# Performance work log

Hardware: AMD Instinct MI355X
Metric: run time of the kernel (lower is better)

## Reference

```python
import jax, jax.numpy as jnp
import numpy as np

B, N, C, E = 8, 4096, 128, 131072  # batch, nodes, channels (in==out), edges


def _linear_params(key, fan_in, fan_out):
    kw, kb = jax.random.split(key)
    s = 1.0 / np.sqrt(fan_in).astype(np.float32)
    W = jax.random.uniform(kw, (fan_in, fan_out), jnp.float32, -s, s)
    b = jax.random.uniform(kb, (fan_out,), jnp.float32, -s, s)
    return W, b


def setup_inputs() -> dict:
    key = jax.random.key(0)
    ks = jax.random.split(key, 6)
    x = jax.random.normal(ks[0], (B, N, C), jnp.float32)
    edge_index = jax.random.randint(ks[1], (2, E), 0, N, jnp.int64)
    W0, b0 = _linear_params(ks[2], C, C)        # lin0: in -> out
    W1, b1 = _linear_params(ks[3], 2 * C, C)    # lin1: 2*out -> out
    W2, b2 = _linear_params(ks[4], C, C)        # lin2: out -> out
    Wo, bo = _linear_params(ks[5], C, C)        # output: out -> out
    return {"x": x, "edge_index": edge_index, "W0": W0, "b0": b0,
            "W1": W1, "b1": b1, "W2": W2, "b2": b2, "Wo": Wo, "bo": bo}


def reference(x, edge_index, W0, b0, W1, b1, W2, b2, Wo, bo):
    n = x.shape[1]
    # symmetric 0/1 adjacency (duplicate edges collapse via .set), zero diagonal
    adj = jnp.zeros((n, n), x.dtype)
    adj = adj.at[edge_index[0], edge_index[1]].set(1.0)
    adj = adj.at[edge_index[1], edge_index[0]].set(1.0)
    diag = jnp.arange(n)
    adj = adj.at[diag, diag].set(0.0)
    h = x @ W0 + b0                               # [B, N, C]
    agg = jnp.einsum('ij,bjd->bid', adj, h)       # neighbor aggregation
    cat = jnp.concatenate([x, agg], axis=-1)      # [B, N, 2C]
    out = (cat @ W1 + b1) @ W2 + b2
    out = jax.nn.gelu(out, approximate=False) @ Wo + bo  # torch exact GELU
    return x + out
```

## Files before the change

### kernel.cpp

```cpp
#include <hip/hip_runtime.h>
#include <hip/hip_bf16.h>
#include <math.h>

#define NN 4096
#define BB 8
#define CC 128
#define EE 131072
#define M_ROWS (BB*NN)
#define DEG_CAP 512

typedef __attribute__((ext_vector_type(8))) short short8;
typedef __attribute__((ext_vector_type(4))) float f32x4;

__device__ __forceinline__ float bf2f(unsigned int u){
    union { unsigned int i; float f; } v; v.i = u << 16; return v.f;
}
__device__ __forceinline__ unsigned short f2bf(float f){
    union { float f; unsigned int i; } v; v.f = f;
    unsigned int u = v.i;
    unsigned int r = u + 0x7FFFu + ((u >> 16) & 1u);
    return (unsigned short)(r >> 16);
}

__device__ __forceinline__ int swz(int r, int k2 ){
    return r * 256 + (k2 ^ ((r & 7) << 4));
}

__global__ __launch_bounds__(256) void k_prep_w(const float* __restrict__ W0, const float* __restrict__ W1,
                                                const float* __restrict__ W2, const float* __restrict__ Wo,
                                                unsigned short* __restrict__ Wt0, unsigned short* __restrict__ Wt1a,
                                                unsigned short* __restrict__ Wt1b, unsigned short* __restrict__ Wt2,
                                                unsigned short* __restrict__ Wto){
    int idx = blockIdx.x * blockDim.x + threadIdx.x;
    int s = idx >> 14;
    int e = idx & 16383;
    int n = e >> 7, k = e & 127;
    float v; unsigned short* dst;
    switch (s){
        case 0:  v = W0[k*128+n];        dst = Wt0;  break;
        case 1:  v = W1[k*128+n];        dst = Wt1a; break;
        case 2:  v = W1[(128+k)*128+n];  dst = Wt1b; break;
        case 3:  v = W2[k*128+n];        dst = Wt2;  break;
        default: v = Wo[k*128+n];        dst = Wto;  break;
    }
    dst[n*128+k] = f2bf(v);
}

__global__ __launch_bounds__(256) void k_scatter(const int* __restrict__ ei,
                                                 unsigned char* __restrict__ adj){
    int e = blockIdx.x * blockDim.x + threadIdx.x;
    if (e < EE){
        int u = ei[e], v = ei[EE + e];
        adj[(size_t)u * NN + v] = 1;
        adj[(size_t)v * NN + u] = 1;
    }
}

__global__ __launch_bounds__(256) void k_csr(const unsigned char* __restrict__ adj,
                                             int* __restrict__ cols, int* __restrict__ deg){
    __shared__ int sc[256];
    int i = blockIdx.x, t = threadIdx.x;
    uint4 w = *((const uint4*)(adj + (size_t)i * NN + t * 16));
    unsigned char b[16]; *((uint4*)b) = w;
    int c = 0;
    #pragma unroll
    for (int q = 0; q < 16; q++){ int j = t*16 + q; if (b[q] && j != i) c++; }
    sc[t] = c; __syncthreads();
    int val = c;
    for (int off = 1; off < 256; off <<= 1){
        int add = (t >= off) ? sc[t - off] : 0;
        __syncthreads();
        val += add; sc[t] = val;
        __syncthreads();
    }
    int total = sc[255];
    int pos = val - c;
    #pragma unroll
    for (int q = 0; q < 16; q++){
        int j = t*16 + q;
        if (b[q] && j != i){
            if (pos < DEG_CAP) cols[(size_t)i * DEG_CAP + pos] = j;
            pos++;
        }
    }
    if (t == 0) deg[i] = total < DEG_CAP ? total : DEG_CAP;
}

__global__ __launch_bounds__(256) void k_agg(const unsigned short* __restrict__ hT,
                                             const int* __restrict__ cols,
                                             const int* __restrict__ deg,
                                             unsigned short* __restrict__ aggbf){
    int i = blockIdx.x, t = threadIdx.x;
    int d = deg[i];
    const int* cl = cols + (size_t)i * DEG_CAP;
    const unsigned short* hp = hT + t * 4;
    float a0 = 0.f, a1 = 0.f, a2 = 0.f, a3 = 0.f;
    int n = 0;
    for (; n + 3 < d; n += 4){
        int4 c = *((const int4*)(cl + n));
        uint2 u0 = *((const uint2*)(hp + ((size_t)c.x << 10)));
        uint2 u1 = *((const uint2*)(hp + ((size_t)c.y << 10)));
        uint2 u2 = *((const uint2*)(hp + ((size_t)c.z << 10)));
        uint2 u3 = *((const uint2*)(hp + ((size_t)c.w << 10)));
        a0 += bf2f(u0.x & 0xFFFFu) + bf2f(u1.x & 0xFFFFu) + bf2f(u2.x & 0xFFFFu) + bf2f(u3.x & 0xFFFFu);
        a1 += bf2f(u0.x >> 16)     + bf2f(u1.x >> 16)     + bf2f(u2.x >> 16)     + bf2f(u3.x >> 16);
        a2 += bf2f(u0.y & 0xFFFFu) + bf2f(u1.y & 0xFFFFu) + bf2f(u2.y & 0xFFFFu) + bf2f(u3.y & 0xFFFFu);
        a3 += bf2f(u0.y >> 16)     + bf2f(u1.y >> 16)     + bf2f(u2.y >> 16)     + bf2f(u3.y >> 16);
    }
    for (; n < d; ++n){
        int j0 = cl[n];
        uint2 u0 = *((const uint2*)(hp + ((size_t)j0 << 10)));
        a0 += bf2f(u0.x & 0xFFFFu);
        a1 += bf2f(u0.x >> 16);
        a2 += bf2f(u0.y & 0xFFFFu);
        a3 += bf2f(u0.y >> 16);
    }
    int b  = t >> 5;
    int ch = (t & 31) * 4;
    ushort4 o; o.x = f2bf(a0); o.y = f2bf(a1); o.z = f2bf(a2); o.w = f2bf(a3);
    *((ushort4*)(aggbf + (size_t)b * (NN*128) + (size_t)i * 128 + ch)) = o;
}

__device__ __forceinline__ void stage_a_bf16(const unsigned short* __restrict__ src, int blockRow,
                                             unsigned short* As, int t){
    #pragma unroll
    for (int it = 0; it < 4; ++it){
        int g = it * 2048 + t * 8;
        int r = g >> 7, k = g & 127;
        uint4 v = *((const uint4*)(src + (size_t)(blockRow + r) * 128 + k));
        *((uint4*)((char*)As + swz(r, k * 2))) = v;
    }
}
__device__ __forceinline__ void stage_a_f32(const float* __restrict__ src, int blockRow,
                                            unsigned short* As, int t){
    #pragma unroll
    for (int it = 0; it < 4; ++it){
        int g = it * 2048 + t * 8;
        int r = g >> 7, k = g & 127;
        const float* p = src + (size_t)(blockRow + r) * 128 + k;
        float4 lo = *((const float4*)p);
        float4 hi = *((const float4*)(p + 4));
        ushort4 w0, w1;
        w0.x = f2bf(lo.x); w0.y = f2bf(lo.y); w0.z = f2bf(lo.z); w0.w = f2bf(lo.w);
        w1.x = f2bf(hi.x); w1.y = f2bf(hi.y); w1.z = f2bf(hi.z); w1.w = f2bf(hi.w);
        char* dst = (char*)As + swz(r, k * 2);
        *((ushort4*)dst) = w0;
        *((ushort4*)(dst + 8)) = w1;
    }
}
__device__ __forceinline__ void stage_w(const unsigned short* __restrict__ Wt,
                                        unsigned short* Ws, int t){
    #pragma unroll
    for (int it = 0; it < 8; ++it){
        int g = it * 2048 + t * 8;
        int r = g >> 7, k = g & 127;
        uint4 v = *((const uint4*)(Wt + r * 128 + k));
        *((uint4*)((char*)Ws + swz(r, k * 2))) = v;
    }
}
__device__ __forceinline__ void mfma_pass(const unsigned short* As, const unsigned short* Ws,
                                          int wr, int wc, int l15, int lh, f32x4 acc[2][4]){
    #pragma unroll
    for (int ks = 0; ks < 4; ++ks){
        const int kc = ks * 32 + lh * 8;
        short8 af[2], bfv[4];
        #pragma unroll
        for (int m = 0; m < 2; m++){
            int r = wr + m * 16 + l15;
            af[m] = *((const short8*)((const char*)As + swz(r, kc * 2)));
        }
        #pragma unroll
        for (int n = 0; n < 4; n++){
            int r = wc + n * 16 + l15;
            bfv[n] = *((const short8*)((const char*)Ws + swz(r, kc * 2)));
        }
        #pragma unroll
        for (int m = 0; m < 2; m++)
            #pragma unroll
            for (int n = 0; n < 4; n++)
                acc[m][n] = __builtin_amdgcn_mfma_f32_16x16x32_bf16(af[m], bfv[n], acc[m][n], 0, 0, 0);
    }
}

__global__ __launch_bounds__(256) void k_gemm0(const float* __restrict__ x,
                                               const unsigned short* __restrict__ Wt0,
                                               const float* __restrict__ b0,
                                               unsigned short* __restrict__ hT){
    __shared__ unsigned short As[64*128];
    __shared__ unsigned short Ws[128*128];
    const int t = threadIdx.x;
    const int blockRow = blockIdx.x * 64;
    stage_a_f32(x, blockRow, As, t);
    stage_w(Wt0, Ws, t);
    __syncthreads();
    const int lane = t & 63, w = t >> 6;
    const int wr = (w >> 1) * 32, wc = (w & 1) * 64;
    const int l15 = lane & 15, lh = lane >> 4;
    f32x4 acc[2][4];
    #pragma unroll
    for (int m = 0; m < 2; m++) for (int n = 0; n < 4; n++) acc[m][n] = (f32x4)(0.0f);
    mfma_pass(As, Ws, wr, wc, l15, lh, acc);
    #pragma unroll
    for (int m = 0; m < 2; m++){
        #pragma unroll
        for (int rr = 0; rr < 4; rr++){
            int row = blockRow + wr + m * 16 + lh * 4 + rr;
            int b_ = row >> 12, j = row & 4095;
            #pragma unroll
            for (int n = 0; n < 4; n++){
                int col = wc + n * 16 + l15;
                float v = acc[m][n][rr] + b0[col];
                hT[(size_t)j * 1024 + b_ * 128 + col] = f2bf(v);
            }
        }
    }
}

__global__ __launch_bounds__(256) void k_gemm1(const float* __restrict__ x,
                                               const unsigned short* __restrict__ agg,
                                               const unsigned short* __restrict__ Wt1a,
                                               const unsigned short* __restrict__ Wt1b,
                                               const float* __restrict__ b1,
                                               unsigned short* __restrict__ t1bf){
    __shared__ unsigned short As[64*128];
    __shared__ unsigned short Ws[128*128];
    const int t = threadIdx.x;
    const int blockRow = blockIdx.x * 64;
    const int lane = t & 63, w = t >> 6;
    const int wr = (w >> 1) * 32, wc = (w & 1) * 64;
    const int l15 = lane & 15, lh = lane >> 4;
    f32x4 acc[2][4];
    #pragma unroll
    for (int m = 0; m < 2; m++) for (int n = 0; n < 4; n++) acc[m][n] = (f32x4)(0.0f);

    stage_a_f32(x, blockRow, As, t);
    stage_w(Wt1a, Ws, t);
    __syncthreads();
    mfma_pass(As, Ws, wr, wc, l15, lh, acc);
    __syncthreads();
    stage_a_bf16(agg, blockRow, As, t);
    stage_w(Wt1b, Ws, t);
    __syncthreads();
    mfma_pass(As, Ws, wr, wc, l15, lh, acc);

    #pragma unroll
    for (int m = 0; m < 2; m++){
        #pragma unroll
        for (int rr = 0; rr < 4; rr++){
            int row = blockRow + wr + m * 16 + lh * 4 + rr;
            #pragma unroll
            for (int n = 0; n < 4; n++){
                int col = wc + n * 16 + l15;
                float v = acc[m][n][rr] + b1[col];
                t1bf[(size_t)row * 128 + col] = f2bf(v);
            }
        }
    }
}

__global__ __launch_bounds__(256) void k_gemm23(const unsigned short* __restrict__ t1bf,
                                                const unsigned short* __restrict__ Wt2,
                                                const unsigned short* __restrict__ Wto,
                                                const float* __restrict__ b2,
                                                const float* __restrict__ bo,
                                                const float* __restrict__ x,
                                                float* __restrict__ out){
    __shared__ unsigned short As[64*128];
    __shared__ unsigned short Ws2[128*128];
    __shared__ unsigned short Wso[128*128];
    const int t = threadIdx.x;
    const int blockRow = blockIdx.x * 64;
    const int lane = t & 63, w = t >> 6;
    const int wr = (w >> 1) * 32, wc = (w & 1) * 64;
    const int l15 = lane & 15, lh = lane >> 4;

    stage_a_bf16(t1bf, blockRow, As, t);
    stage_w(Wt2, Ws2, t);
    stage_w(Wto, Wso, t);
    __syncthreads();

    f32x4 acc[2][4];
    #pragma unroll
    for (int m = 0; m < 2; m++) for (int n = 0; n < 4; n++) acc[m][n] = (f32x4)(0.0f);
    mfma_pass(As, Ws2, wr, wc, l15, lh, acc);
    __syncthreads();

    #pragma unroll
    for (int m = 0; m < 2; m++){
        #pragma unroll
        for (int rr = 0; rr < 4; rr++){
            int rl = wr + m * 16 + lh * 4 + rr;
            #pragma unroll
            for (int n = 0; n < 4; n++){
                int col = wc + n * 16 + l15;
                float v = acc[m][n][rr] + b2[col];
                v = 0.5f * v * (1.0f + erff(v * 0.70710678118f));
                *((unsigned short*)((char*)As + swz(rl, col * 2))) = f2bf(v);
            }
        }
    }
    __syncthreads();

    f32x4 acc2[2][4];
    #pragma unroll
    for (int m = 0; m < 2; m++) for (int n = 0; n < 4; n++) acc2[m][n] = (f32x4)(0.0f);
    mfma_pass(As, Wso, wr, wc, l15, lh, acc2);

    #pragma unroll
    for (int m = 0; m < 2; m++){
        #pragma unroll
        for (int rr = 0; rr < 4; rr++){
            int row = blockRow + wr + m * 16 + lh * 4 + rr;
            #pragma unroll
            for (int n = 0; n < 4; n++){
                int col = wc + n * 16 + l15;
                float v = acc2[m][n][rr] + bo[col] + x[(size_t)row * 128 + col];
                out[(size_t)row * 128 + col] = v;
            }
        }
    }
}

extern "C" void kernel_launch(void* const* d_in, const int* in_sizes, int n_in,
                              void* d_out, int out_size, void* d_ws, size_t ws_size,
                              hipStream_t stream) {
    const float* x  = (const float*)d_in[0];
    const int*   ei = (const int*)d_in[1];
    const float* W0 = (const float*)d_in[2];
    const float* b0 = (const float*)d_in[3];
    const float* W1 = (const float*)d_in[4];
    const float* b1 = (const float*)d_in[5];
    const float* W2 = (const float*)d_in[6];
    const float* b2 = (const float*)d_in[7];
    const float* Wo = (const float*)d_in[8];
    const float* bo = (const float*)d_in[9];
    float* out = (float*)d_out;

    char* ws = (char*)d_ws;
    unsigned char* adj   = (unsigned char*)(ws + 0);
    int*   cols          = (int*)(ws + 16777216);
    int*   deg           = (int*)(ws + 25165824);
    unsigned short* hT   = (unsigned short*)(ws + 25182208);
    unsigned short* aggb = (unsigned short*)(ws + 33570816);
    unsigned short* t1bf = (unsigned short*)(ws + 41959424);
    unsigned short* Wt0  = (unsigned short*)(ws + 50348032);
    unsigned short* Wt1a = (unsigned short*)(ws + 50348032 + 32768);
    unsigned short* Wt1b = (unsigned short*)(ws + 50348032 + 65536);
    unsigned short* Wt2  = (unsigned short*)(ws + 50348032 + 98304);
    unsigned short* Wto  = (unsigned short*)(ws + 50348032 + 131072);

    hipMemsetAsync(adj, 0, (size_t)NN * NN, stream);

    k_prep_w<<<320, 256, 0, stream>>>(W0, W1, W2, Wo, Wt0, Wt1a, Wt1b, Wt2, Wto);
    k_scatter<<<EE / 256, 256, 0, stream>>>(ei, adj);
    k_csr<<<NN, 256, 0, stream>>>(adj, cols, deg);

    k_gemm0<<<M_ROWS / 64, 256, 0, stream>>>(x, Wt0, b0, hT);
    k_agg<<<NN, 256, 0, stream>>>(hT, cols, deg, aggb);
    k_gemm1<<<M_ROWS / 64, 256, 0, stream>>>(x, aggb, Wt1a, Wt1b, b1, t1bf);
    k_gemm23<<<M_ROWS / 64, 256, 0, stream>>>(t1bf, Wt2, Wto, b2, bo, x, out);
}
```

Baseline: 93.80 us.

## Use bitset adjacency with atomicOr and widen aggregation loads

Replaces the 16 MB byte adjacency matrix with a 2 MB bitset built via atomicOr, so the memset and the CSR pass read far less memory; CSR build now uses popcount and ffs over 32-bit words. The aggregation kernel stages column indices in shared memory, uses 16-byte loads covering 8 channels per thread, splits neighbors across two thread halves, and reduces through shared memory. Atomics add contention on the scatter step, and the extra sync and reduction add overhead in the aggregation kernel.

```diff
diff --git a/kernel.cpp b/kernel.cpp
--- a/kernel.cpp
+++ b/kernel.cpp
@@ -47,78 +47,98 @@
 }
 
 __global__ __launch_bounds__(256) void k_scatter(const int* __restrict__ ei,
-                                                 unsigned char* __restrict__ adj){
+                                                 unsigned int* __restrict__ bits){
     int e = blockIdx.x * blockDim.x + threadIdx.x;
     if (e < EE){
         int u = ei[e], v = ei[EE + e];
-        adj[(size_t)u * NN + v] = 1;
-        adj[(size_t)v * NN + u] = 1;
-    }
-}
-
-__global__ __launch_bounds__(256) void k_csr(const unsigned char* __restrict__ adj,
+        atomicOr(&bits[u * 128 + (v >> 5)], 1u << (v & 31));
+        atomicOr(&bits[v * 128 + (u >> 5)], 1u << (u & 31));
+    }
+}
+
+__global__ __launch_bounds__(128) void k_csr(const unsigned int* __restrict__ bits,
                                              int* __restrict__ cols, int* __restrict__ deg){
-    __shared__ int sc[256];
+    __shared__ int sc[128];
     int i = blockIdx.x, t = threadIdx.x;
-    uint4 w = *((const uint4*)(adj + (size_t)i * NN + t * 16));
-    unsigned char b[16]; *((uint4*)b) = w;
-    int c = 0;
-    #pragma unroll
-    for (int q = 0; q < 16; q++){ int j = t*16 + q; if (b[q] && j != i) c++; }
+    unsigned int w = bits[i * 128 + t];
+    if (t == (i >> 5)) w &= ~(1u << (i & 31));
+    int c = __popc(w);
     sc[t] = c; __syncthreads();
     int val = c;
-    for (int off = 1; off < 256; off <<= 1){
+    for (int off = 1; off < 128; off <<= 1){
         int add = (t >= off) ? sc[t - off] : 0;
         __syncthreads();
         val += add; sc[t] = val;
         __syncthreads();
     }
-    int total = sc[255];
+    int total = sc[127];
     int pos = val - c;
-    #pragma unroll
-    for (int q = 0; q < 16; q++){
-        int j = t*16 + q;
-        if (b[q] && j != i){
-            if (pos < DEG_CAP) cols[(size_t)i * DEG_CAP + pos] = j;
-            pos++;
-        }
+    unsigned int ww = w;
+    while (ww){
+        int b = __ffs(ww) - 1;
+        ww &= ww - 1;
+        if (pos < DEG_CAP) cols[(size_t)i * DEG_CAP + pos] = t * 32 + b;
+        pos++;
     }
     if (t == 0) deg[i] = total < DEG_CAP ? total : DEG_CAP;
+}
+
+__device__ __forceinline__ void acc8(uint4 u, float* a){
+    a[0] += bf2f(u.x & 0xFFFFu); a[1] += bf2f(u.x >> 16);
+    a[2] += bf2f(u.y & 0xFFFFu); a[3] += bf2f(u.y >> 16);
+    a[4] += bf2f(u.z & 0xFFFFu); a[5] += bf2f(u.z >> 16);
+    a[6] += bf2f(u.w & 0xFFFFu); a[7] += bf2f(u.w >> 16);
 }
 
 __global__ __launch_bounds__(256) void k_agg(const unsigned short* __restrict__ hT,
                                              const int* __restrict__ cols,
                                              const int* __restrict__ deg,
                                              unsigned short* __restrict__ aggbf){
-    int i = blockIdx.x, t = threadIdx.x;
-    int d = deg[i];
+    __shared__ int scol[DEG_CAP];
+    __shared__ float red[128][9];
+    const int i = blockIdx.x, t = threadIdx.x;
+    const int half = t >> 7, lane = t & 127;
+    const int d = deg[i];
     const int* cl = cols + (size_t)i * DEG_CAP;
-    const unsigned short* hp = hT + t * 4;
-    float a0 = 0.f, a1 = 0.f, a2 = 0.f, a3 = 0.f;
-    int n = 0;
-    for (; n + 3 < d; n += 4){
-        int4 c = *((const int4*)(cl + n));
-        uint2 u0 = *((const uint2*)(hp + ((size_t)c.x << 10)));
-        uint2 u1 = *((const uint2*)(hp + ((size_t)c.y << 10)));
-        uint2 u2 = *((const uint2*)(hp + ((size_t)c.z << 10)));
-        uint2 u3 = *((const uint2*)(hp + ((size_t)c.w << 10)));
-        a0 += bf2f(u0.x & 0xFFFFu) + bf2f(u1.x & 0xFFFFu) + bf2f(u2.x & 0xFFFFu) + bf2f(u3.x & 0xFFFFu);
-        a1 += bf2f(u0.x >> 16)     + bf2f(u1.x >> 16)     + bf2f(u2.x >> 16)     + bf2f(u3.x >> 16);
-        a2 += bf2f(u0.y & 0xFFFFu) + bf2f(u1.y & 0xFFFFu) + bf2f(u2.y & 0xFFFFu) + bf2f(u3.y & 0xFFFFu);
-        a3 += bf2f(u0.y >> 16)     + bf2f(u1.y >> 16)     + bf2f(u2.y >> 16)     + bf2f(u3.y >> 16);
-    }
-    for (; n < d; ++n){
-        int j0 = cl[n];
-        uint2 u0 = *((const uint2*)(hp + ((size_t)j0 << 10)));
-        a0 += bf2f(u0.x & 0xFFFFu);
-        a1 += bf2f(u0.x >> 16);
-        a2 += bf2f(u0.y & 0xFFFFu);
-        a3 += bf2f(u0.y >> 16);
-    }
-    int b  = t >> 5;
-    int ch = (t & 31) * 4;
-    ushort4 o; o.x = f2bf(a0); o.y = f2bf(a1); o.z = f2bf(a2); o.w = f2bf(a3);
-    *((ushort4*)(aggbf + (size_t)b * (NN*128) + (size_t)i * 128 + ch)) = o;
+    for (int q = t; q < d; q += 256) scol[q] = cl[q];
+    __syncthreads();
+
+    const unsigned short* hp = hT + lane * 8;
+    float a[8];
+    #pragma unroll
+    for (int c = 0; c < 8; c++) a[c] = 0.f;
+
+    int n = half;
+    for (; n + 6 < d; n += 8){
+        int j0 = scol[n], j1 = scol[n+2], j2 = scol[n+4], j3 = scol[n+6];
+        uint4 u0 = *((const uint4*)(hp + ((size_t)j0 << 10)));
+        uint4 u1 = *((const uint4*)(hp + ((size_t)j1 << 10)));
+        uint4 u2 = *((const uint4*)(hp + ((size_t)j2 << 10)));
+        uint4 u3 = *((const uint4*)(hp + ((size_t)j3 << 10)));
+        acc8(u0, a); acc8(u1, a); acc8(u2, a); acc8(u3, a);
+    }
+    for (; n < d; n += 2){
+        uint4 u0 = *((const uint4*)(hp + ((size_t)scol[n] << 10)));
+        acc8(u0, a);
+    }
+
+    if (half){
+        #pragma unroll
+        for (int c = 0; c < 8; c++) red[lane][c] = a[c];
+    }
+    __syncthreads();
+    if (!half){
+        #pragma unroll
+        for (int c = 0; c < 8; c++) a[c] += red[lane][c];
+        int b  = lane >> 4;
+        int ch = (lane * 8) & 127;
+        uint4 o;
+        o.x = (unsigned)f2bf(a[0]) | ((unsigned)f2bf(a[1]) << 16);
+        o.y = (unsigned)f2bf(a[2]) | ((unsigned)f2bf(a[3]) << 16);
+        o.z = (unsigned)f2bf(a[4]) | ((unsigned)f2bf(a[5]) << 16);
+        o.w = (unsigned)f2bf(a[6]) | ((unsigned)f2bf(a[7]) << 16);
+        *((uint4*)(aggbf + (size_t)b * (NN*128) + (size_t)i * 128 + ch)) = o;
+    }
 }
 
 __device__ __forceinline__ void stage_a_bf16(const unsigned short* __restrict__ src, int blockRow,
@@ -337,23 +357,23 @@
     float* out = (float*)d_out;
 
     char* ws = (char*)d_ws;
-    unsigned char* adj   = (unsigned char*)(ws + 0);
-    int*   cols          = (int*)(ws + 16777216);
-    int*   deg           = (int*)(ws + 25165824);
-    unsigned short* hT   = (unsigned short*)(ws + 25182208);
-    unsigned short* aggb = (unsigned short*)(ws + 33570816);
-    unsigned short* t1bf = (unsigned short*)(ws + 41959424);
-    unsigned short* Wt0  = (unsigned short*)(ws + 50348032);
-    unsigned short* Wt1a = (unsigned short*)(ws + 50348032 + 32768);
-    unsigned short* Wt1b = (unsigned short*)(ws + 50348032 + 65536);
-    unsigned short* Wt2  = (unsigned short*)(ws + 50348032 + 98304);
-    unsigned short* Wto  = (unsigned short*)(ws + 50348032 + 131072);
-
-    hipMemsetAsync(adj, 0, (size_t)NN * NN, stream);
+    unsigned int* bits   = (unsigned int*)(ws + 0);
+    int*   cols          = (int*)(ws + 2097152);
+    int*   deg           = (int*)(ws + 10485760);
+    unsigned short* hT   = (unsigned short*)(ws + 10502144);
+    unsigned short* aggb = (unsigned short*)(ws + 18890752);
+    unsigned short* t1bf = (unsigned short*)(ws + 27279360);
+    unsigned short* Wt0  = (unsigned short*)(ws + 35667968);
+    unsigned short* Wt1a = (unsigned short*)(ws + 35667968 + 32768);
+    unsigned short* Wt1b = (unsigned short*)(ws + 35667968 + 65536);
+    unsigned short* Wt2  = (unsigned short*)(ws + 35667968 + 98304);
+    unsigned short* Wto  = (unsigned short*)(ws + 35667968 + 131072);
+
+    hipMemsetAsync(bits, 0, 2097152, stream);
 
     k_prep_w<<<320, 256, 0, stream>>>(W0, W1, W2, Wo, Wt0, Wt1a, Wt1b, Wt2, Wto);
-    k_scatter<<<EE / 256, 256, 0, stream>>>(ei, adj);
-    k_csr<<<NN, 256, 0, stream>>>(adj, cols, deg);
+    k_scatter<<<EE / 256, 256, 0, stream>>>(ei, bits);
+    k_csr<<<NN, 128, 0, stream>>>(bits, cols, deg);
 
     k_gemm0<<<M_ROWS / 64, 256, 0, stream>>>(x, Wt0, b0, hT);
     k_agg<<<NN, 256, 0, stream>>>(hT, cols, deg, aggb);
```

New measurement: 93.37 us. No clear change (-0.5%).
